# Performance work log

Hardware: AMD Instinct MI355X
Metric: run time of the kernel (lower is better)

Reference implementation:

```python
import jax, jax.numpy as jnp
import numpy as np

B, T, F, H = 4096, 60, 128, 256

def setup_inputs() -> dict:
    key = jax.random.key(0)
    ks = jax.random.split(key, 14)
    sk = 1.0 / np.sqrt(H)
    def unif(k, shape):
        return jax.random.uniform(k, shape, jnp.float32, -sk, sk)
    return {
        "x": jax.random.normal(ks[0], (B, T, F), jnp.float32),
        "Wf": unif(ks[1], (F + H, H)), "bf": unif(ks[2], (H,)),
        "Wu": unif(ks[3], (F + H, H)), "bu": unif(ks[4], (H,)),
        "Wc": unif(ks[5], (F + H, H)), "bc": unif(ks[6], (H,)),
        "Wo": unif(ks[7], (F + H, H)), "bo": unif(ks[8], (H,)),
        "Wd1": jax.random.normal(ks[9], (H, H), jnp.float32) * np.sqrt(2.0 / H),
        "bd1": jnp.zeros((H,), jnp.float32),
        "Wd2": jax.random.normal(ks[10], (H, 1), jnp.float32) * np.sqrt(2.0 / H),
        "bd2": jnp.zeros((1,), jnp.float32),
    }

def reference(x, Wf, bf, Wu, bu, Wc, bc, Wo, bo, Wd1, bd1, Wd2, bd2):
    b = x.shape[0]
    h0 = jnp.zeros((b, H), x.dtype)
    c0 = jnp.zeros((b, H), x.dtype)

    def step(carry, xt):
        h, c = carry
        z = jnp.concatenate([xt, h], axis=-1)  # [B, F+H]
        f = jax.nn.sigmoid(z @ Wf + bf)
        u = jax.nn.sigmoid(z @ Wu + bu)
        g = jnp.tanh(z @ Wc + bc)
        o = jax.nn.sigmoid(z @ Wo + bo)
        c_new = f * c + u * g
        h_new = o * jnp.tanh(c_new)
        return (h_new, c_new), None

    (h, _), _ = jax.lax.scan(step, (h0, c0), jnp.swapaxes(x, 0, 1))  # scan over T
    # dense head: two stacked linear layers, no intermediate activation
    out = (h @ Wd1 + bd1) @ Wd2 + bd2  # [B, 1]
    return out
```

## Files before the change

kernel.cpp:

```cpp
#include <hip/hip_runtime.h>


#define T_STEPS 60
#define F_DIM 128
#define H_DIM 256
#define BC 16
#define ZQ 31.75f
#define L2E 1.44269504f

typedef __attribute__((ext_vector_type(4))) int intx4;

__device__ __forceinline__ int q8(float v) {
    return __float2int_rn(fminf(fmaxf(v, -127.f), 127.f));
}

__global__ __launch_bounds__(1024)
void prep_kernel(const float* __restrict__ Wf, const float* __restrict__ Wu,
                 const float* __restrict__ Wc, const float* __restrict__ Wo,
                 const float* __restrict__ Wd1, const float* __restrict__ bd1,
                 const float* __restrict__ Wd2, const float* __restrict__ bd2,
                 float* __restrict__ cscale, intx4* __restrict__ qpack,
                 float* __restrict__ vhead, float* __restrict__ shead) {
    const int t = threadIdx.x;
    const int b = blockIdx.x;
    if (b < 8) {
        __shared__ float red[16][128];
        __shared__ float fsc[128];
        const int g = b >> 1, ch = b & 1;
        const float* W = (g == 0) ? Wf : (g == 1) ? Wu : (g == 2) ? Wc : Wo;
        const int col = ch * 128 + (t & 127);
        const int grp = t >> 7;
        float mx = 1e-20f, mh = 1e-20f;
#pragma unroll 4
        for (int i = 0; i < 16; ++i)
            mx = fmaxf(mx, fabsf(W[(size_t)(grp * 16 + i) * H_DIM + col]));
#pragma unroll 4
        for (int i = 0; i < 32; ++i)
            mh = fmaxf(mh, fabsf(W[(size_t)(128 + grp * 32 + i) * H_DIM + col]));
        red[grp][t & 127] = mx;
        red[8 + grp][t & 127] = mh;
        __syncthreads();
        if (t < 128) {
            float Mx = red[0][t], Mh = red[8][t];
#pragma unroll
            for (int i = 1; i < 8; ++i) {
                Mx = fmaxf(Mx, red[i][t]);
                Mh = fmaxf(Mh, red[8 + i][t]);
            }
            float cs = fmaxf(4.f * Mx, Mh) * (1.f / 16129.f);
            cscale[g * 256 + ch * 128 + t] = cs;
            fsc[t] = 1.f / (127.f * cs);
        }
        __syncthreads();
#pragma unroll
        for (int i = 0; i < 3; ++i) {
            int task = i * 1024 + t;
            int lane = task & 63, fr = task >> 6;
            int hl = fr / 6, ks6 = fr - hl * 6;
            int l15 = lane & 15, quad = lane >> 4;
            int colw = ch * 128 + hl * 16 + l15;
            int k0 = ks6 * 64 + quad * 16;
            float f = ((ks6 < 2) ? 4.f : 1.f) * fsc[hl * 16 + l15];
            int w[4];
#pragma unroll
            for (int d = 0; d < 4; ++d) {
                int b0 = q8(W[(size_t)(k0 + d * 4 + 0) * H_DIM + colw] * f) & 255;
                int b1 = q8(W[(size_t)(k0 + d * 4 + 1) * H_DIM + colw] * f) & 255;
                int b2 = q8(W[(size_t)(k0 + d * 4 + 2) * H_DIM + colw] * f) & 255;
                int b3 = q8(W[(size_t)(k0 + d * 4 + 3) * H_DIM + colw] * f) & 255;
                w[d] = b0 | (b1 << 8) | (b2 << 16) | (b3 << 24);
            }
            intx4 v = {w[0], w[1], w[2], w[3]};
            qpack[(((ch * 8 + hl) * 4 + g) * 6 + ks6) * 64 + lane] = v;
        }
    } else {
        __shared__ float hp[1024];
        const int j = t >> 2, q = t & 3;
        float s = 0.f;
        const float* row = Wd1 + (size_t)j * H_DIM + q * 64;
#pragma unroll
        for (int i = 0; i < 16; ++i) {
            float4 a = *(const float4*)(row + i * 4);
            float4 bb = *(const float4*)(Wd2 + q * 64 + i * 4);
            s += a.x * bb.x + a.y * bb.y + a.z * bb.z + a.w * bb.w;
        }
        hp[t] = s;
        __syncthreads();
        float vj = 0.f;
        if (q == 0) vj = hp[t] + hp[t + 1] + hp[t + 2] + hp[t + 3];
        __syncthreads();
        if (q == 0) vhead[j] = vj;
        if (t < 256) hp[t] = bd1[t] * Wd2[t];
        __syncthreads();
        for (int off = 128; off > 0; off >>= 1) {
            if (t < off) hp[t] += hp[t + off];
            __syncthreads();
        }
        if (t == 0) shead[0] = hp[0] + bd2[0];
    }
}

__global__ __launch_bounds__(512)
__attribute__((amdgpu_waves_per_eu(2, 2)))
void lstm_kernel(const float* __restrict__ x,
                 const float* __restrict__ bfv, const float* __restrict__ buv,
                 const float* __restrict__ bcv, const float* __restrict__ bov,
                 const intx4* __restrict__ qpack,
                 const float* __restrict__ cscale,
                 const float* __restrict__ vhead, const float* __restrict__ shead,
                 float* __restrict__ out)
{
    __shared__ __align__(16) intx4 wlds[64 * 64];
    __shared__ __align__(16) signed char zbuf[2][6][1024];
    __shared__ float rowsum[BC];

    const int tid  = threadIdx.x;
    const int wave = tid >> 6;
    const int lane = tid & 63;
    const int quad = lane >> 4;
    const int l15  = lane & 15;
    const int b0   = blockIdx.x * BC;

    for (int i = tid; i < 64 * 64; i += 512)
        wlds[i] = qpack[((i >> 6) * 6 + 5) * 64 + (i & 63)];
    intx4 wreg[5][8];
#pragma unroll
    for (int j = 0; j < 8; ++j)
#pragma unroll
        for (int ks = 0; ks < 5; ++ks) {
            intx4 v = qpack[(((8 * wave + j) * 6 + ks) * 64) + lane];
            int a0 = v[0], a1 = v[1], a2 = v[2], a3 = v[3];
            asm volatile("" : "+v"(a0), "+v"(a1), "+v"(a2), "+v"(a3));
            intx4 w = {a0, a1, a2, a3};
            wreg[ks][j] = w;
        }

    for (int i = tid; i < 2 * 6 * 1024 / 4; i += 512) ((int*)zbuf)[i] = 0;
    if (tid < BC) rowsum[tid] = 0.f;

    float csS[2][4], bS[2][4], vh[2];
    float creg[2][4] = {};
    int haddr[2];
#pragma unroll
    for (int hb = 0; hb < 2; ++hb) {
        int a = 2 * wave + hb;
        int hc = a * 16 + l15;
        vh[hb] = vhead[hc];
        haddr[hb] = (2 + (a >> 2)) * 1024 + (a & 3) * 256 + l15;
#pragma unroll
        for (int g = 0; g < 4; ++g) {
            float cs = cscale[g * 256 + hc];
            float bi = (g == 0 ? bfv : g == 1 ? buv : g == 2 ? bcv : bov)[hc];
            float m = (g == 2) ? (-2.f * L2E) : (-L2E);
            csS[hb][g] = m * cs;
            bS[hb][g] = m * bi;
        }
    }

    const int xm = tid >> 5, xi = tid & 31;
    const int f0 = xi * 4;
    const int xaddr = (f0 >> 6) * 1024 + ((f0 & 63) >> 4) * 256 + xm * 16 + (f0 & 15);
    const float* xp = x + (size_t)(b0 + xm) * T_STEPS * F_DIM + f0;

    __syncthreads();
    float4 xv = *(const float4*)(xp);
    {
        unsigned u = (unsigned)(q8(xv.x * ZQ) & 255) | ((unsigned)(q8(xv.y * ZQ) & 255) << 8) |
                     ((unsigned)(q8(xv.z * ZQ) & 255) << 16) | ((unsigned)(q8(xv.w * ZQ) & 255) << 24);
        *(unsigned*)(&zbuf[0][0][0] + xaddr) = u;
    }
    xv = *(const float4*)(xp + F_DIM);
    __syncthreads();

#define GATE_CELL(hb, rr)                                                          \
    {                                                                              \
        float uf = fmaf((float)acc[(hb) * 4 + 0][rr], csS[hb][0], bS[hb][0]);      \
        float uu = fmaf((float)acc[(hb) * 4 + 1][rr], csS[hb][1], bS[hb][1]);      \
        float uc = fmaf((float)acc[(hb) * 4 + 2][rr], csS[hb][2], bS[hb][2]);      \
        float uo = fmaf((float)acc[(hb) * 4 + 3][rr], csS[hb][3], bS[hb][3]);      \
        float af = 1.f + __builtin_amdgcn_exp2f(uf);                               \
        float au = 1.f + __builtin_amdgcn_exp2f(uu);                               \
        float ac = 1.f + __builtin_amdgcn_exp2f(uc);                               \
        float ao = 1.f + __builtin_amdgcn_exp2f(uo);                               \
        float r1 = __builtin_amdgcn_rcpf(af * au);                                 \
        float r2 = __builtin_amdgcn_rcpf(ac * ao);                                 \
        float fg = au * r1;                                                        \
        float ug = af * r1;                                                        \
        float rc = ao * r2;                                                        \
        float og = ac * r2;                                                        \
        float cn = fmaf(fg, creg[hb][rr], fmaf(ug + ug, rc, -ug));                 \
        creg[hb][rr] = cn;                                                         \
        float rh = __builtin_amdgcn_rcpf(1.f + __builtin_amdgcn_exp2f(cn * (-2.f * L2E))); \
        float hn = fmaf(og + og, rh, -og);                                         \
        zw[haddr[hb] + (quad * 4 + (rr)) * 16] =                                   \
            (signed char)__float2int_rn(hn * 127.f);                               \
    }

#pragma unroll 1
    for (int t = 0; t < T_STEPS - 1; ++t) {
        const int p = t & 1;
        const intx4* zr = (const intx4*)(&zbuf[p][0][0]);
        signed char* zw = &zbuf[p ^ 1][0][0];

        intx4 acc[8] = {};

#pragma unroll
        for (int ks = 0; ks < 6; ++ks) {
            intx4 a = zr[ks * 64 + lane];
            if (ks < 5) {
#pragma unroll
                for (int j = 0; j < 4; ++j)
                    acc[j] = __builtin_amdgcn_mfma_i32_16x16x64_i8(a, wreg[ks][j], acc[j], 0, 0, 0);
            } else {
#pragma unroll
                for (int j = 0; j < 4; ++j)
                    acc[j] = __builtin_amdgcn_mfma_i32_16x16x64_i8(
                        a, wlds[(8 * wave + j) * 64 + lane], acc[j], 0, 0, 0);
            }
        }

        {
            unsigned u = (unsigned)(q8(xv.x * ZQ) & 255) | ((unsigned)(q8(xv.y * ZQ) & 255) << 8) |
                         ((unsigned)(q8(xv.z * ZQ) & 255) << 16) | ((unsigned)(q8(xv.w * ZQ) & 255) << 24);
            *(unsigned*)(zw + xaddr) = u;
            int tn = (t + 2 < T_STEPS) ? (t + 2) : (T_STEPS - 1);
            xv = *(const float4*)(xp + (size_t)tn * F_DIM);
        }

#pragma unroll
        for (int ks = 0; ks < 6; ++ks) {
            intx4 a = zr[ks * 64 + lane];
            if (ks < 5) {
#pragma unroll
                for (int j = 4; j < 8; ++j)
                    acc[j] = __builtin_amdgcn_mfma_i32_16x16x64_i8(a, wreg[ks][j], acc[j], 0, 0, 0);
            } else {
#pragma unroll
                for (int j = 4; j < 8; ++j)
                    acc[j] = __builtin_amdgcn_mfma_i32_16x16x64_i8(
                        a, wlds[(8 * wave + j) * 64 + lane], acc[j], 0, 0, 0);
            }
            if (ks >= 1 && ks < 5) GATE_CELL(0, ks - 1);
        }
        GATE_CELL(1, 0);
        GATE_CELL(1, 1);
        GATE_CELL(1, 2);
        GATE_CELL(1, 3);

        __syncthreads();
    }

    {
        const intx4* zr = (const intx4*)(&zbuf[(T_STEPS - 1) & 1][0][0]);
        intx4 acc[8] = {};
#pragma unroll
        for (int ks = 0; ks < 5; ++ks) {
            intx4 a = zr[ks * 64 + lane];
#pragma unroll
            for (int j = 0; j < 8; ++j)
                acc[j] = __builtin_amdgcn_mfma_i32_16x16x64_i8(a, wreg[ks][j], acc[j], 0, 0, 0);
        }
        {
            intx4 a5 = zr[5 * 64 + lane];
#pragma unroll
            for (int j = 0; j < 8; ++j) {
                intx4 bw = wlds[(8 * wave + j) * 64 + lane];
                acc[j] = __builtin_amdgcn_mfma_i32_16x16x64_i8(a5, bw, acc[j], 0, 0, 0);
            }
        }
        float hs[4] = {0.f, 0.f, 0.f, 0.f};
#pragma unroll
        for (int hb = 0; hb < 2; ++hb)
#pragma unroll
            for (int rr = 0; rr < 4; ++rr) {
                float uf = fmaf((float)acc[hb * 4 + 0][rr], csS[hb][0], bS[hb][0]);
                float uu = fmaf((float)acc[hb * 4 + 1][rr], csS[hb][1], bS[hb][1]);
                float uc = fmaf((float)acc[hb * 4 + 2][rr], csS[hb][2], bS[hb][2]);
                float uo = fmaf((float)acc[hb * 4 + 3][rr], csS[hb][3], bS[hb][3]);
                float af = 1.f + __builtin_amdgcn_exp2f(uf);
                float au = 1.f + __builtin_amdgcn_exp2f(uu);
                float ac = 1.f + __builtin_amdgcn_exp2f(uc);
                float ao = 1.f + __builtin_amdgcn_exp2f(uo);
                float r1 = __builtin_amdgcn_rcpf(af * au);
                float r2 = __builtin_amdgcn_rcpf(ac * ao);
                float fg = au * r1;
                float ug = af * r1;
                float rc = ao * r2;
                float og = ac * r2;
                float cn = fmaf(fg, creg[hb][rr], fmaf(ug + ug, rc, -ug));
                float rh = __builtin_amdgcn_rcpf(1.f + __builtin_amdgcn_exp2f(cn * (-2.f * L2E)));
                float hn = fmaf(og + og, rh, -og);
                hs[rr] += hn * vh[hb];
            }
#pragma unroll
        for (int rr = 0; rr < 4; ++rr) {
            float s = hs[rr];
#pragma unroll
            for (int m = 1; m < 16; m <<= 1)
                s += __shfl_xor(s, m, 64);
            if (l15 == 0)
                atomicAdd(&rowsum[quad * 4 + rr], s);
        }
        __syncthreads();
    }
#undef GATE_CELL

    if (tid < BC)
        out[b0 + tid] = rowsum[tid] + shead[0];
}

extern "C" void kernel_launch(void* const* d_in, const int* in_sizes, int n_in,
                              void* d_out, int out_size, void* d_ws, size_t ws_size,
                              hipStream_t stream) {
    (void)in_sizes; (void)n_in; (void)out_size; (void)ws_size;
    const float* x   = (const float*)d_in[0];
    const float* Wf  = (const float*)d_in[1];
    const float* bfv = (const float*)d_in[2];
    const float* Wu  = (const float*)d_in[3];
    const float* buv = (const float*)d_in[4];
    const float* Wc  = (const float*)d_in[5];
    const float* bcv = (const float*)d_in[6];
    const float* Wo  = (const float*)d_in[7];
    const float* bov = (const float*)d_in[8];
    const float* Wd1 = (const float*)d_in[9];
    const float* bd1 = (const float*)d_in[10];
    const float* Wd2 = (const float*)d_in[11];
    const float* bd2 = (const float*)d_in[12];

    char* ws = (char*)d_ws;
    intx4* qpack = (intx4*)ws;
    size_t off = (size_t)384 * 64 * 16;
    float* cscale = (float*)(ws + off); off += 1024 * 4;
    float* vhead  = (float*)(ws + off); off += 256 * 4;
    float* shead  = (float*)(ws + off); off += 16;

    prep_kernel<<<9, 1024, 0, stream>>>(Wf, Wu, Wc, Wo, Wd1, bd1, Wd2, bd2,
                                        cscale, qpack, vhead, shead);
    lstm_kernel<<<256, 512, 0, stream>>>(x, bfv, buv, bcv, bov, qpack, cscale,
                                         vhead, shead, (float*)d_out);
}
```

Before: 316.3 us.

## Pre-quantize x to int8 in prep kernel and simplify LSTM step loop

The prep kernel now spreads weight quantization over 32 blocks instead of 8. When the workspace is large enough, extra blocks also quantize all of x to packed int8 ahead of time, so the LSTM kernel streams a quarter of the bytes per timestep and skips the per-step conversion. The recurrent loop is also restructured: the split MFMA halves with interleaved gate math are replaced by one full MFMA pass followed by the gate computations, and the last step is folded into the loop. The trade-offs are an extra full pass over x in global memory before the recurrence and the loss of the earlier overlap between MFMA and gate arithmetic.

After: 334.1 us. 1.06x slower.

```diff
diff --git a/kernel.cpp b/kernel.cpp
--- a/kernel.cpp
+++ b/kernel.cpp
@@ -4,6 +4,7 @@
 #define T_STEPS 60
 #define F_DIM 128
 #define H_DIM 256
+#define B_DIM 4096
 #define BC 16
 #define ZQ 31.75f
 #define L2E 1.44269504f
@@ -20,47 +21,48 @@
                  const float* __restrict__ Wd1, const float* __restrict__ bd1,
                  const float* __restrict__ Wd2, const float* __restrict__ bd2,
                  float* __restrict__ cscale, intx4* __restrict__ qpack,
-                 float* __restrict__ vhead, float* __restrict__ shead) {
+                 float* __restrict__ vhead, float* __restrict__ shead,
+                 const float* __restrict__ x, unsigned* __restrict__ qx) {
     const int t = threadIdx.x;
     const int b = blockIdx.x;
-    if (b < 8) {
-        __shared__ float red[16][128];
-        __shared__ float fsc[128];
-        const int g = b >> 1, ch = b & 1;
+    if (b < 32) {
+        __shared__ float red[64][32];
+        __shared__ float fsc[32];
+        const int g = b >> 3, ch = (b >> 2) & 1, qtr = b & 3;
         const float* W = (g == 0) ? Wf : (g == 1) ? Wu : (g == 2) ? Wc : Wo;
-        const int col = ch * 128 + (t & 127);
-        const int grp = t >> 7;
+        const int c32 = t & 31;
+        const int col = ch * 128 + qtr * 32 + c32;
+        const int grp = t >> 5;
         float mx = 1e-20f, mh = 1e-20f;
-#pragma unroll 4
-        for (int i = 0; i < 16; ++i)
-            mx = fmaxf(mx, fabsf(W[(size_t)(grp * 16 + i) * H_DIM + col]));
-#pragma unroll 4
-        for (int i = 0; i < 32; ++i)
-            mh = fmaxf(mh, fabsf(W[(size_t)(128 + grp * 32 + i) * H_DIM + col]));
-        red[grp][t & 127] = mx;
-        red[8 + grp][t & 127] = mh;
-        __syncthreads();
-        if (t < 128) {
-            float Mx = red[0][t], Mh = red[8][t];
-#pragma unroll
-            for (int i = 1; i < 8; ++i) {
+#pragma unroll
+        for (int i = 0; i < 4; ++i)
+            mx = fmaxf(mx, fabsf(W[(size_t)(grp * 4 + i) * H_DIM + col]));
+#pragma unroll
+        for (int i = 0; i < 8; ++i)
+            mh = fmaxf(mh, fabsf(W[(size_t)(128 + grp * 8 + i) * H_DIM + col]));
+        red[grp][c32] = mx;
+        red[32 + grp][c32] = mh;
+        __syncthreads();
+        if (t < 32) {
+            float Mx = red[0][t], Mh = red[32][t];
+#pragma unroll 8
+            for (int i = 1; i < 32; ++i) {
                 Mx = fmaxf(Mx, red[i][t]);
-                Mh = fmaxf(Mh, red[8 + i][t]);
+                Mh = fmaxf(Mh, red[32 + i][t]);
             }
             float cs = fmaxf(4.f * Mx, Mh) * (1.f / 16129.f);
-            cscale[g * 256 + ch * 128 + t] = cs;
+            cscale[g * 256 + ch * 128 + qtr * 32 + t] = cs;
             fsc[t] = 1.f / (127.f * cs);
         }
         __syncthreads();
-#pragma unroll
-        for (int i = 0; i < 3; ++i) {
-            int task = i * 1024 + t;
-            int lane = task & 63, fr = task >> 6;
-            int hl = fr / 6, ks6 = fr - hl * 6;
+        if (t < 768) {
+            int lane = t & 63, fr = t >> 6;
+            int hli = fr / 6, ks6 = fr - hli * 6;
+            int hl = qtr * 2 + hli;
             int l15 = lane & 15, quad = lane >> 4;
             int colw = ch * 128 + hl * 16 + l15;
             int k0 = ks6 * 64 + quad * 16;
-            float f = ((ks6 < 2) ? 4.f : 1.f) * fsc[hl * 16 + l15];
+            float f = ((ks6 < 2) ? 4.f : 1.f) * fsc[hli * 16 + l15];
             int w[4];
 #pragma unroll
             for (int d = 0; d < 4; ++d) {
@@ -73,7 +75,7 @@
             intx4 v = {w[0], w[1], w[2], w[3]};
             qpack[(((ch * 8 + hl) * 4 + g) * 6 + ks6) * 64 + lane] = v;
         }
-    } else {
+    } else if (b == 32) {
         __shared__ float hp[1024];
         const int j = t >> 2, q = t & 3;
         float s = 0.f;
@@ -97,9 +99,21 @@
             __syncthreads();
         }
         if (t == 0) shead[0] = hp[0] + bd2[0];
+    } else {
+        const size_t NW = (size_t)B_DIM * T_STEPS * (F_DIM / 4);
+        const size_t stride = (size_t)(gridDim.x - 33) * 1024;
+        for (size_t w = (size_t)(b - 33) * 1024 + t; w < NW; w += stride) {
+            float4 v = *(const float4*)(x + w * 4);
+            unsigned u = (unsigned)(q8(v.x * ZQ) & 255) |
+                         ((unsigned)(q8(v.y * ZQ) & 255) << 8) |
+                         ((unsigned)(q8(v.z * ZQ) & 255) << 16) |
+                         ((unsigned)(q8(v.w * ZQ) & 255) << 24);
+            qx[w] = u;
+        }
     }
 }
 
+template <bool USE_QX>
 __global__ __launch_bounds__(512)
 __attribute__((amdgpu_waves_per_eu(2, 2)))
 void lstm_kernel(const float* __restrict__ x,
@@ -108,6 +122,7 @@
                  const intx4* __restrict__ qpack,
                  const float* __restrict__ cscale,
                  const float* __restrict__ vhead, const float* __restrict__ shead,
+                 const unsigned* __restrict__ qx,
                  float* __restrict__ out)
 {
     __shared__ __align__(16) intx4 wlds[64 * 64];
@@ -161,15 +176,22 @@
     const int f0 = xi * 4;
     const int xaddr = (f0 >> 6) * 1024 + ((f0 & 63) >> 4) * 256 + xm * 16 + (f0 & 15);
     const float* xp = x + (size_t)(b0 + xm) * T_STEPS * F_DIM + f0;
+    const unsigned* qxp = qx + (size_t)(b0 + xm) * T_STEPS * (F_DIM / 4) + xi;
 
     __syncthreads();
-    float4 xv = *(const float4*)(xp);
-    {
+    float4 xv;
+    unsigned xu;
+    if constexpr (USE_QX) {
+        unsigned u0 = qxp[0];
+        *(unsigned*)(&zbuf[0][0][0] + xaddr) = u0;
+        xu = qxp[32];
+    } else {
+        xv = *(const float4*)(xp);
         unsigned u = (unsigned)(q8(xv.x * ZQ) & 255) | ((unsigned)(q8(xv.y * ZQ) & 255) << 8) |
                      ((unsigned)(q8(xv.z * ZQ) & 255) << 16) | ((unsigned)(q8(xv.w * ZQ) & 255) << 24);
         *(unsigned*)(&zbuf[0][0][0] + xaddr) = u;
-    }
-    xv = *(const float4*)(xp + F_DIM);
+        xv = *(const float4*)(xp + F_DIM);
+    }
     __syncthreads();
 
 #define GATE_CELL(hb, rr)                                                          \
@@ -196,62 +218,11 @@
             (signed char)__float2int_rn(hn * 127.f);                               \
     }
 
-#pragma unroll 1
-    for (int t = 0; t < T_STEPS - 1; ++t) {
-        const int p = t & 1;
+    for (int t = 0; t < T_STEPS; ++t) {
+        const int p = t & 1, pn = p ^ 1;
         const intx4* zr = (const intx4*)(&zbuf[p][0][0]);
-        signed char* zw = &zbuf[p ^ 1][0][0];
-
-        intx4 acc[8] = {};
-
-#pragma unroll
-        for (int ks = 0; ks < 6; ++ks) {
-            intx4 a = zr[ks * 64 + lane];
-            if (ks < 5) {
-#pragma unroll
-                for (int j = 0; j < 4; ++j)
-                    acc[j] = __builtin_amdgcn_mfma_i32_16x16x64_i8(a, wreg[ks][j], acc[j], 0, 0, 0);
-            } else {
-#pragma unroll
-                for (int j = 0; j < 4; ++j)
-                    acc[j] = __builtin_amdgcn_mfma_i32_16x16x64_i8(
-                        a, wlds[(8 * wave + j) * 64 + lane], acc[j], 0, 0, 0);
-            }
-        }
-
-        {
-            unsigned u = (unsigned)(q8(xv.x * ZQ) & 255) | ((unsigned)(q8(xv.y * ZQ) & 255) << 8) |
-                         ((unsigned)(q8(xv.z * ZQ) & 255) << 16) | ((unsigned)(q8(xv.w * ZQ) & 255) << 24);
-            *(unsigned*)(zw + xaddr) = u;
-            int tn = (t + 2 < T_STEPS) ? (t + 2) : (T_STEPS - 1);
-            xv = *(const float4*)(xp + (size_t)tn * F_DIM);
-        }
-
-#pragma unroll
-        for (int ks = 0; ks < 6; ++ks) {
-            intx4 a = zr[ks * 64 + lane];
-            if (ks < 5) {
-#pragma unroll
-                for (int j = 4; j < 8; ++j)
-                    acc[j] = __builtin_amdgcn_mfma_i32_16x16x64_i8(a, wreg[ks][j], acc[j], 0, 0, 0);
-            } else {
-#pragma unroll
-                for (int j = 4; j < 8; ++j)
-                    acc[j] = __builtin_amdgcn_mfma_i32_16x16x64_i8(
-                        a, wlds[(8 * wave + j) * 64 + lane], acc[j], 0, 0, 0);
-            }
-            if (ks >= 1 && ks < 5) GATE_CELL(0, ks - 1);
-        }
-        GATE_CELL(1, 0);
-        GATE_CELL(1, 1);
-        GATE_CELL(1, 2);
-        GATE_CELL(1, 3);
-
-        __syncthreads();
-    }
-
-    {
-        const intx4* zr = (const intx4*)(&zbuf[(T_STEPS - 1) & 1][0][0]);
+        signed char* zw = &zbuf[pn][0][0];
+
         intx4 acc[8] = {};
 #pragma unroll
         for (int ks = 0; ks < 5; ++ks) {
@@ -268,38 +239,59 @@
                 acc[j] = __builtin_amdgcn_mfma_i32_16x16x64_i8(a5, bw, acc[j], 0, 0, 0);
             }
         }
-        float hs[4] = {0.f, 0.f, 0.f, 0.f};
-#pragma unroll
-        for (int hb = 0; hb < 2; ++hb)
+
+        if (t < T_STEPS - 1) {
+            if constexpr (USE_QX) {
+                *(unsigned*)(zw + xaddr) = xu;
+                if (t < T_STEPS - 2)
+                    xu = qxp[(size_t)(t + 2) * 32];
+            } else {
+                unsigned u = (unsigned)(q8(xv.x * ZQ) & 255) | ((unsigned)(q8(xv.y * ZQ) & 255) << 8) |
+                             ((unsigned)(q8(xv.z * ZQ) & 255) << 16) | ((unsigned)(q8(xv.w * ZQ) & 255) << 24);
+                *(unsigned*)(zw + xaddr) = u;
+                if (t < T_STEPS - 2)
+                    xv = *(const float4*)(xp + (size_t)(t + 2) * F_DIM);
+            }
+
+#pragma unroll
+            for (int hb = 0; hb < 2; ++hb)
+#pragma unroll
+                for (int rr = 0; rr < 4; ++rr)
+                    GATE_CELL(hb, rr);
+        } else {
+            float hs[4] = {0.f, 0.f, 0.f, 0.f};
+#pragma unroll
+            for (int hb = 0; hb < 2; ++hb)
+#pragma unroll
+                for (int rr = 0; rr < 4; ++rr) {
+                    float uf = fmaf((float)acc[hb * 4 + 0][rr], csS[hb][0], bS[hb][0]);
+                    float uu = fmaf((float)acc[hb * 4 + 1][rr], csS[hb][1], bS[hb][1]);
+                    float uc = fmaf((float)acc[hb * 4 + 2][rr], csS[hb][2], bS[hb][2]);
+                    float uo = fmaf((float)acc[hb * 4 + 3][rr], csS[hb][3], bS[hb][3]);
+                    float af = 1.f + __builtin_amdgcn_exp2f(uf);
+                    float au = 1.f + __builtin_amdgcn_exp2f(uu);
+                    float ac = 1.f + __builtin_amdgcn_exp2f(uc);
+                    float ao = 1.f + __builtin_amdgcn_exp2f(uo);
+                    float r1 = __builtin_amdgcn_rcpf(af * au);
+                    float r2 = __builtin_amdgcn_rcpf(ac * ao);
+                    float fg = au * r1;
+                    float ug = af * r1;
+                    float rc = ao * r2;
+                    float og = ac * r2;
+                    float cn = fmaf(fg, creg[hb][rr], fmaf(ug + ug, rc, -ug));
+                    float rh = __builtin_amdgcn_rcpf(1.f + __builtin_amdgcn_exp2f(cn * (-2.f * L2E)));
+                    float hn = fmaf(og + og, rh, -og);
+                    hs[rr] += hn * vh[hb];
+                }
 #pragma unroll
             for (int rr = 0; rr < 4; ++rr) {
-                float uf = fmaf((float)acc[hb * 4 + 0][rr], csS[hb][0], bS[hb][0]);
-                float uu = fmaf((float)acc[hb * 4 + 1][rr], csS[hb][1], bS[hb][1]);
-                float uc = fmaf((float)acc[hb * 4 + 2][rr], csS[hb][2], bS[hb][2]);
-                float uo = fmaf((float)acc[hb * 4 + 3][rr], csS[hb][3], bS[hb][3]);
-                float af = 1.f + __builtin_amdgcn_exp2f(uf);
-                float au = 1.f + __builtin_amdgcn_exp2f(uu);
-                float ac = 1.f + __builtin_amdgcn_exp2f(uc);
-                float ao = 1.f + __builtin_amdgcn_exp2f(uo);
-                float r1 = __builtin_amdgcn_rcpf(af * au);
-                float r2 = __builtin_amdgcn_rcpf(ac * ao);
-                float fg = au * r1;
-                float ug = af * r1;
-                float rc = ao * r2;
-                float og = ac * r2;
-                float cn = fmaf(fg, creg[hb][rr], fmaf(ug + ug, rc, -ug));
-                float rh = __builtin_amdgcn_rcpf(1.f + __builtin_amdgcn_exp2f(cn * (-2.f * L2E)));
-                float hn = fmaf(og + og, rh, -og);
-                hs[rr] += hn * vh[hb];
-            }
-#pragma unroll
-        for (int rr = 0; rr < 4; ++rr) {
-            float s = hs[rr];
-#pragma unroll
-            for (int m = 1; m < 16; m <<= 1)
-                s += __shfl_xor(s, m, 64);
-            if (l15 == 0)
-                atomicAdd(&rowsum[quad * 4 + rr], s);
+                float s = hs[rr];
+#pragma unroll
+                for (int m = 1; m < 16; m <<= 1)
+                    s += __shfl_xor(s, m, 64);
+                if (l15 == 0)
+                    atomicAdd(&rowsum[quad * 4 + rr], s);
+            }
         }
         __syncthreads();
     }
@@ -312,7 +304,7 @@
 extern "C" void kernel_launch(void* const* d_in, const int* in_sizes, int n_in,
                               void* d_out, int out_size, void* d_ws, size_t ws_size,
                               hipStream_t stream) {
-    (void)in_sizes; (void)n_in; (void)out_size; (void)ws_size;
+    (void)in_sizes; (void)n_in; (void)out_size;
     const float* x   = (const float*)d_in[0];
     const float* Wf  = (const float*)d_in[1];
     const float* bfv = (const float*)d_in[2];
@@ -333,9 +325,18 @@
     float* cscale = (float*)(ws + off); off += 1024 * 4;
     float* vhead  = (float*)(ws + off); off += 256 * 4;
     float* shead  = (float*)(ws + off); off += 16;
-
-    prep_kernel<<<9, 1024, 0, stream>>>(Wf, Wu, Wc, Wo, Wd1, bd1, Wd2, bd2,
-                                        cscale, qpack, vhead, shead);
-    lstm_kernel<<<256, 512, 0, stream>>>(x, bfv, buv, bcv, bov, qpack, cscale,
-                                         vhead, shead, (float*)d_out);
+    unsigned* qx  = (unsigned*)(ws + off);
+    const size_t qx_bytes = (size_t)B_DIM * T_STEPS * (F_DIM / 4) * 4;
+    const bool use_qx = ws_size >= off + qx_bytes;
+
+    prep_kernel<<<use_qx ? 545 : 33, 1024, 0, stream>>>(
+        Wf, Wu, Wc, Wo, Wd1, bd1, Wd2, bd2, cscale, qpack, vhead, shead, x, qx);
+    if (use_qx)
+        lstm_kernel<true><<<256, 512, 0, stream>>>(x, bfv, buv, bcv, bov, qpack,
+                                                   cscale, vhead, shead, qx,
+                                                   (float*)d_out);
+    else
+        lstm_kernel<false><<<256, 512, 0, stream>>>(x, bfv, buv, bcv, bov, qpack,
+                                                    cscale, vhead, shead, qx,
+                                                    (float*)d_out);
 }
```
